# Optimization experiments

Hardware: AMD Instinct MI355X
Metric: run time of the kernel (lower is better)

## Reference

```python
import jax, jax.numpy as jnp
import numpy as np
import math

E = 1024   # embed_dim
H = 16     # num_heads
LAT = 1024 # latent_dim
P = LAT // 16  # projectionMatrice output dim (per-head width)
B = 2
S = 2048


def setup_inputs() -> dict:
    key = jax.random.key(0)
    ks = jax.random.split(key, 11)
    sc = 0.02  # small init scale so exp(dot(q_vec, k_vec)) stays finite
    return {
        "x": jax.random.normal(ks[0], (B, S, E), jnp.float32),
        "WQ": jax.random.normal(ks[1], (E, E), jnp.float32) * sc,
        "WK": jax.random.normal(ks[2], (E, E), jnp.float32) * sc,
        "WV": jax.random.normal(ks[3], (E, E), jnp.float32) * sc,
        "result_weight": jax.random.normal(ks[4], (E, E), jnp.float32) * sc,
        "proj_w": jax.random.normal(ks[5], (E, P), jnp.float32) * sc,
        "proj_b": jax.random.normal(ks[6], (P,), jnp.float32) * sc,
        "q1_vector": jax.random.normal(ks[7], (E,), jnp.float32) * sc,
        "k1_vector": jax.random.normal(ks[8], (E,), jnp.float32) * sc,
        "q2_vector": jax.random.normal(ks[9], (E,), jnp.float32) * sc,
        "k2_vector": jax.random.normal(ks[10], (E,), jnp.float32) * sc,
        "lambda_init": jnp.zeros((1,), jnp.float32),
    }


def reference(x, WQ, WK, WV, result_weight, proj_w, proj_b,
              q1_vector, k1_vector, q2_vector, k2_vector, lambda_init):
    head_dim = E // H
    scale = 1.0 / math.sqrt(head_dim)
    # projectionMatrice(x @ W): torch Linear -> x @ proj_w + proj_b with proj_w [E, P]
    q = (x @ WQ) @ proj_w + proj_b   # [B, S, P]
    k = (x @ WK) @ proj_w + proj_b   # [B, S, P]
    v = (x @ WV) @ proj_w + proj_b   # [B, S, P]
    q1, q2 = jnp.split(q, 2, axis=-1)  # [B, S, P/2] each
    k1, k2 = jnp.split(k, 2, axis=-1)
    lam = (jnp.exp(jnp.dot(q1_vector, k1_vector))
           - jnp.exp(jnp.dot(q2_vector, k2_vector)) + lambda_init[0])
    attn1 = jnp.einsum('bsp,btp->bst', q1, k1) * scale  # [B, S, S]
    attn2 = jnp.einsum('bsp,btp->bst', q2, k2) * scale
    base = jnp.einsum('bst,btp->bsp', attn1 - lam * attn2, v)  # [B, S, P]
    # Stateful KV-cache grows by one identical (key, value) copy per head call;
    # head i's tiled-cache output equals (i+1) * base (exact reassociation).
    mult = jnp.arange(1, H + 1, dtype=x.dtype)  # [H]
    heads = (base[:, :, None, :] * mult[None, None, :, None]).reshape(B, S, H * P)  # [B, S, E]
    return heads @ result_weight
```

## Files before the change

kernel.cpp:

```cpp
#include <hip/hip_runtime.h>
#include <hip/hip_bf16.h>


typedef __attribute__((ext_vector_type(8))) short short8;
typedef __attribute__((ext_vector_type(4))) float f32x4;
typedef unsigned short ushort_t;
typedef unsigned int uint_t;

__device__ inline ushort_t f2bf(float v) {
    uint_t u = __float_as_uint(v);
    return (ushort_t)((u + 0x7FFF + ((u >> 16) & 1)) >> 16);
}
__device__ inline float bf2f(ushort_t h) { return __uint_as_float(((uint_t)h) << 16); }
__device__ inline void split2(float v, ushort_t& hi, ushort_t& lo) {
    hi = f2bf(v);
    lo = f2bf(v - bf2f(hi));
}
__device__ inline int swzA(int row, int k) { return (row * 64 + k) ^ ((row & 7) << 3); }

__global__ __launch_bounds__(256) void prep2(
    const float* __restrict__ WQ, const float* __restrict__ WK, const float* __restrict__ WV,
    const float* __restrict__ proj_w, const float* __restrict__ RW,
    const float* __restrict__ q1v, const float* __restrict__ k1v,
    const float* __restrict__ q2v, const float* __restrict__ k2v,
    const float* __restrict__ lam0,
    ushort_t* __restrict__ WpThi, ushort_t* __restrict__ WpTlo,
    float* __restrict__ Weff, float* __restrict__ lamOut)
{
    int bid = blockIdx.x, tid = threadIdx.x;
    if (bid < 48) {
        __shared__ __align__(16) ushort_t Ah[4096], Al[4096], Bh[4096], Bl[4096];
        int z = bid >> 4, icb = bid & 15;
        const float* Wz = (z == 0) ? WQ : (z == 1) ? WK : WV;
        int i0 = icb * 64;
        int wave = tid >> 6, lane = tid & 63, rl = lane & 15, kg = lane >> 4;
        f32x4 acc[4] = {};
        float4 av[4], bv[4];
        #pragma unroll
        for (int i = 0; i < 4; ++i) {
            int pos = tid + 256 * i;
            int r = pos >> 4, c4 = (pos & 15) * 4;
            av[i] = *(const float4*)&proj_w[(long long)r * 64 + c4];
            bv[i] = *(const float4*)&Wz[(long long)(i0 + r) * 1024 + c4];
        }
        for (int ch = 0; ch < 16; ++ch) {
            #pragma unroll
            for (int i = 0; i < 4; ++i) {
                int pos = tid + 256 * i;
                int r = pos >> 4, c4 = (pos & 15) * 4;
                float va[4] = {av[i].x, av[i].y, av[i].z, av[i].w};
                #pragma unroll
                for (int j = 0; j < 4; ++j) {
                    ushort_t h, l; split2(va[j], h, l);
                    int idx = swzA(c4 + j, r);
                    Ah[idx] = h; Al[idx] = l;
                }
                ushort4 h4, l4;
                split2(bv[i].x, h4.x, l4.x); split2(bv[i].y, h4.y, l4.y);
                split2(bv[i].z, h4.z, l4.z); split2(bv[i].w, h4.w, l4.w);
                int bi = swzA(r, c4);
                *(ushort4*)&Bh[bi] = h4;
                *(ushort4*)&Bl[bi] = l4;
            }
            __syncthreads();
            if (ch < 15) {
                int k0 = (ch + 1) * 64;
                #pragma unroll
                for (int i = 0; i < 4; ++i) {
                    int pos = tid + 256 * i;
                    int r = pos >> 4, c4 = (pos & 15) * 4;
                    av[i] = *(const float4*)&proj_w[(long long)(k0 + r) * 64 + c4];
                    bv[i] = *(const float4*)&Wz[(long long)(i0 + r) * 1024 + k0 + c4];
                }
            }
            int ar = wave * 16 + rl;
            #pragma unroll
            for (int ks = 0; ks < 2; ++ks) {
                int kb = ks * 32 + kg * 8;
                short8 ah = *(const short8*)&Ah[swzA(ar, kb)];
                short8 al = *(const short8*)&Al[swzA(ar, kb)];
                #pragma unroll
                for (int n = 0; n < 4; ++n) {
                    int bi = swzA(n * 16 + rl, kb);
                    short8 bh = *(const short8*)&Bh[bi];
                    short8 bl = *(const short8*)&Bl[bi];
                    acc[n] = __builtin_amdgcn_mfma_f32_16x16x32_bf16(ah, bh, acc[n], 0, 0, 0);
                    acc[n] = __builtin_amdgcn_mfma_f32_16x16x32_bf16(ah, bl, acc[n], 0, 0, 0);
                    acc[n] = __builtin_amdgcn_mfma_f32_16x16x32_bf16(al, bh, acc[n], 0, 0, 0);
                }
            }
            __builtin_amdgcn_s_barrier();
        }
        #pragma unroll
        for (int n = 0; n < 4; ++n) {
            int icol = i0 + n * 16 + rl;
            #pragma unroll
            for (int j = 0; j < 4; ++j) {
                int prow = wave * 16 + kg * 4 + j;
                ushort_t h, l; split2(acc[n][j], h, l);
                long long idx = (long long)(z * 64 + prow) * 1024 + icol;
                WpThi[idx] = h; WpTlo[idx] = l;
            }
        }
    } else if (bid < 112) {
        int f4i = (bid - 48) * 256 + tid;
        int p = f4i >> 8, e4 = (f4i & 255) * 4;
        float4 s = {0.f, 0.f, 0.f, 0.f};
        #pragma unroll
        for (int h = 0; h < 16; ++h) {
            float4 r = *(const float4*)&RW[(long long)(h * 64 + p) * 1024 + e4];
            float m = (float)(h + 1);
            s.x += m * r.x; s.y += m * r.y; s.z += m * r.z; s.w += m * r.w;
        }
        *(float4*)&Weff[(long long)p * 1024 + e4] = s;
    } else {
        __shared__ float red[2][4];
        float d1 = 0.f, d2 = 0.f;
        for (int i = tid; i < 1024; i += 256) {
            d1 += q1v[i] * k1v[i];
            d2 += q2v[i] * k2v[i];
        }
        #pragma unroll
        for (int off = 32; off > 0; off >>= 1) {
            d1 += __shfl_down(d1, off);
            d2 += __shfl_down(d2, off);
        }
        int wave = tid >> 6;
        if ((tid & 63) == 0) { red[0][wave] = d1; red[1][wave] = d2; }
        __syncthreads();
        if (tid == 0) {
            float s1 = red[0][0] + red[0][1] + red[0][2] + red[0][3];
            float s2 = red[1][0] + red[1][1] + red[1][2] + red[1][3];
            *lamOut = expf(s1) - expf(s2) + lam0[0];
        }
    }
}

__global__ __launch_bounds__(256) void qkv2(
    const float* __restrict__ x,
    const ushort_t* __restrict__ WpThi, const ushort_t* __restrict__ WpTlo,
    const float* __restrict__ proj_b,
    ushort_t* __restrict__ Qhi, ushort_t* __restrict__ Qlo,
    float* __restrict__ kbuf, float* __restrict__ vbuf)
{
    __shared__ __align__(16) ushort_t Ah[4096], Al[4096], Bh[4096], Bl[4096];
    int bid = blockIdx.x, tid = threadIdx.x;
    int z = bid >> 6, rowblk = bid & 63;
    long long row0 = (long long)rowblk * 64;
    int wave = tid >> 6, lane = tid & 63, rl = lane & 15, kg = lane >> 4;
    f32x4 acc[4] = {};
    float4 av[4];
    short8 pbh[2], pbl[2];
    #pragma unroll
    for (int i = 0; i < 4; ++i) {
        int pos = tid + 256 * i;
        int r = pos >> 4, c4 = (pos & 15) * 4;
        av[i] = *(const float4*)&x[(row0 + r) * 1024 + c4];
    }
    #pragma unroll
    for (int i = 0; i < 2; ++i) {
        int pos = tid + 256 * i;
        int n = pos >> 3, k8 = (pos & 7) * 8;
        long long src = (long long)(z * 64 + n) * 1024 + k8;
        pbh[i] = *(const short8*)&WpThi[src];
        pbl[i] = *(const short8*)&WpTlo[src];
    }
    for (int ch = 0; ch < 16; ++ch) {
        #pragma unroll
        for (int i = 0; i < 4; ++i) {
            int pos = tid + 256 * i;
            int r = pos >> 4, c4 = (pos & 15) * 4;
            ushort4 h, l;
            split2(av[i].x, h.x, l.x); split2(av[i].y, h.y, l.y);
            split2(av[i].z, h.z, l.z); split2(av[i].w, h.w, l.w);
            int idx = swzA(r, c4);
            *(ushort4*)&Ah[idx] = h;
            *(ushort4*)&Al[idx] = l;
        }
        #pragma unroll
        for (int i = 0; i < 2; ++i) {
            int pos = tid + 256 * i;
            int n = pos >> 3, k8 = (pos & 7) * 8;
            int idx = swzA(n, k8);
            *(short8*)&Bh[idx] = pbh[i];
            *(short8*)&Bl[idx] = pbl[i];
        }
        __syncthreads();
        if (ch < 15) {
            int k0 = (ch + 1) * 64;
            #pragma unroll
            for (int i = 0; i < 4; ++i) {
                int pos = tid + 256 * i;
                int r = pos >> 4, c4 = (pos & 15) * 4;
                av[i] = *(const float4*)&x[(row0 + r) * 1024 + k0 + c4];
            }
            #pragma unroll
            for (int i = 0; i < 2; ++i) {
                int pos = tid + 256 * i;
                int n = pos >> 3, k8 = (pos & 7) * 8;
                long long src = (long long)(z * 64 + n) * 1024 + k0 + k8;
                pbh[i] = *(const short8*)&WpThi[src];
                pbl[i] = *(const short8*)&WpTlo[src];
            }
        }
        int ar = wave * 16 + rl;
        #pragma unroll
        for (int ks = 0; ks < 2; ++ks) {
            int kb = ks * 32 + kg * 8;
            short8 ah = *(const short8*)&Ah[swzA(ar, kb)];
            short8 al = *(const short8*)&Al[swzA(ar, kb)];
            #pragma unroll
            for (int n = 0; n < 4; ++n) {
                int bi = swzA(n * 16 + rl, kb);
                short8 bh = *(const short8*)&Bh[bi];
                short8 bl = *(const short8*)&Bl[bi];
                acc[n] = __builtin_amdgcn_mfma_f32_16x16x32_bf16(ah, bh, acc[n], 0, 0, 0);
                acc[n] = __builtin_amdgcn_mfma_f32_16x16x32_bf16(ah, bl, acc[n], 0, 0, 0);
                acc[n] = __builtin_amdgcn_mfma_f32_16x16x32_bf16(al, bh, acc[n], 0, 0, 0);
            }
        }
        __builtin_amdgcn_s_barrier();
    }
    #pragma unroll
    for (int n = 0; n < 4; ++n) {
        int col = n * 16 + rl;
        float bb = proj_b[col];
        #pragma unroll
        for (int j = 0; j < 4; ++j) {
            long long row = row0 + wave * 16 + kg * 4 + j;
            float val = acc[n][j] + bb;
            if (z == 0) {
                ushort_t h, l; split2(val, h, l);
                Qhi[row * 64 + col] = h;
                Qlo[row * 64 + col] = l;
            } else if (z == 1) {
                kbuf[row * 64 + col] = val;
            } else {
                vbuf[row * 64 + col] = val;
            }
        }
    }
}

__global__ __launch_bounds__(256) void mpart2(
    const float* __restrict__ kbuf, const float* __restrict__ vbuf,
    float* __restrict__ Mpart)
{
    int bid = blockIdx.x;
    int sc = bid & 63, b = bid >> 6;
    __shared__ float ksh[32][68], vsh[32][68];
    int tid = threadIdx.x;
    long long row0 = (long long)b * 2048 + sc * 32;
    #pragma unroll
    for (int i = 0; i < 4; ++i) {
        int pos = tid + 256 * i;
        int arr = pos >> 9, rem = pos & 511;
        int r = rem >> 4, c4 = (rem & 15) * 4;
        const float* src = (arr ? vbuf : kbuf) + (row0 + r) * 64 + c4;
        float4 v = *(const float4*)src;
        if (arr == 0) *(float4*)&ksh[r][c4] = v;
        else          *(float4*)&vsh[r][c4] = v;
    }
    __syncthreads();
    int p = tid & 63, cg = tid >> 6;
    float acc[16] = {};
    for (int s = 0; s < 32; ++s) {
        float vv = vsh[s][p];
        float4 k0 = *(const float4*)&ksh[s][cg * 16];
        float4 k1 = *(const float4*)&ksh[s][cg * 16 + 4];
        float4 k2 = *(const float4*)&ksh[s][cg * 16 + 8];
        float4 k3 = *(const float4*)&ksh[s][cg * 16 + 12];
        acc[0] += k0.x * vv;  acc[1] += k0.y * vv;  acc[2] += k0.z * vv;  acc[3] += k0.w * vv;
        acc[4] += k1.x * vv;  acc[5] += k1.y * vv;  acc[6] += k1.z * vv;  acc[7] += k1.w * vv;
        acc[8] += k2.x * vv;  acc[9] += k2.y * vv;  acc[10] += k2.z * vv; acc[11] += k2.w * vv;
        acc[12] += k3.x * vv; acc[13] += k3.y * vv; acc[14] += k3.z * vv; acc[15] += k3.w * vv;
    }
    float* o = Mpart + ((long long)b * 64 + sc) * 4096;
    #pragma unroll
    for (int ci = 0; ci < 16; ++ci)
        o[(cg * 16 + ci) * 64 + p] = acc[ci];
}

__global__ __launch_bounds__(256) void meffk(
    const float* __restrict__ Mpart, const float* __restrict__ lamPtr,
    float* __restrict__ Meff)
{
    int idx = blockIdx.x * 256 + threadIdx.x;
    int b = idx >> 12, cp = idx & 4095, c = cp >> 6;
    const float* base = Mpart + (long long)b * 262144 + cp;
    float s = 0.f;
    #pragma unroll 8
    for (int sc = 0; sc < 64; ++sc) s += base[(long long)sc * 4096];
    float lam = *lamPtr;
    Meff[idx] = s * 0.125f * (c < 32 ? 1.0f : -lam);
}

__global__ __launch_bounds__(256) void gkern2(
    const float* __restrict__ Meff, const float* __restrict__ Weff,
    ushort_t* __restrict__ GThi, ushort_t* __restrict__ GTlo)
{
    int colblk = blockIdx.x & 15, b = blockIdx.x >> 4;
    __shared__ float As[64][68];
    __shared__ float Bs[64][68];
    int tid = threadIdx.x;
    #pragma unroll
    for (int i = 0; i < 4; ++i) {
        int pos = tid + 256 * i;
        int c = pos >> 4, p4 = (pos & 15) * 4;
        *(float4*)&As[c][p4] = *(const float4*)&Meff[(long long)b * 4096 + c * 64 + p4];
    }
    #pragma unroll
    for (int i = 0; i < 4; ++i) {
        int pos = tid + 256 * i;
        int kk = pos >> 4, n4 = (pos & 15) * 4;
        *(float4*)&Bs[kk][n4] = *(const float4*)&Weff[(long long)kk * 1024 + colblk * 64 + n4];
    }
    __syncthreads();

    int tx = tid & 15, ty = tid >> 4;
    float acc[4][4] = {};
    #pragma unroll 4
    for (int kk4 = 0; kk4 < 64; kk4 += 4) {
        float4 a4[4], b4[4];
        #pragma unroll
        for (int i = 0; i < 4; ++i) a4[i] = *(const float4*)&As[ty * 4 + i][kk4];
        #pragma unroll
        for (int r = 0; r < 4; ++r) b4[r] = *(const float4*)&Bs[kk4 + r][tx * 4];
        #pragma unroll
        for (int i = 0; i < 4; ++i) {
            acc[i][0] += a4[i].x * b4[0].x + a4[i].y * b4[1].x + a4[i].z * b4[2].x + a4[i].w * b4[3].x;
            acc[i][1] += a4[i].x * b4[0].y + a4[i].y * b4[1].y + a4[i].z * b4[2].y + a4[i].w * b4[3].y;
            acc[i][2] += a4[i].x * b4[0].z + a4[i].y * b4[1].z + a4[i].z * b4[2].z + a4[i].w * b4[3].z;
            acc[i][3] += a4[i].x * b4[0].w + a4[i].y * b4[1].w + a4[i].z * b4[2].w + a4[i].w * b4[3].w;
        }
    }
    #pragma unroll
    for (int i = 0; i < 4; ++i)
        #pragma unroll
        for (int j = 0; j < 4; ++j) {
            ushort_t h, l; split2(acc[i][j], h, l);
            long long idx = (long long)b * 65536 + (long long)(colblk * 64 + tx * 4 + j) * 64 + ty * 4 + i;
            GThi[idx] = h; GTlo[idx] = l;
        }
}

__global__ __launch_bounds__(256) void outk(
    const ushort_t* __restrict__ Qhi, const ushort_t* __restrict__ Qlo,
    const ushort_t* __restrict__ GThi, const ushort_t* __restrict__ GTlo,
    float* __restrict__ out)
{
    __shared__ __align__(16) ushort_t Ah[4096], Al[4096], Bh[4096], Bl[4096];
    int bid = blockIdx.x;
    int rowblk = bid & 31, colblk = (bid >> 5) & 15, b = bid >> 9;
    int tid = threadIdx.x;
    long long row0 = (long long)b * 2048 + rowblk * 64;

    #pragma unroll
    for (int i = 0; i < 2; ++i) {
        int pos = tid + 256 * i;
        int n = pos >> 3, k8 = (pos & 7) * 8;
        int idx = swzA(n, k8);
        long long qsrc = (row0 + n) * 64 + k8;
        long long gsrc = (long long)b * 65536 + (long long)(colblk * 64 + n) * 64 + k8;
        *(short8*)&Ah[idx] = *(const short8*)&Qhi[qsrc];
        *(short8*)&Al[idx] = *(const short8*)&Qlo[qsrc];
        *(short8*)&Bh[idx] = *(const short8*)&GThi[gsrc];
        *(short8*)&Bl[idx] = *(const short8*)&GTlo[gsrc];
    }
    __syncthreads();

    int wave = tid >> 6, lane = tid & 63;
    int rl = lane & 15, kg = lane >> 4;
    f32x4 acc[4] = {};
    int ar = wave * 16 + rl;
    #pragma unroll
    for (int ks = 0; ks < 2; ++ks) {
        int kb = ks * 32 + kg * 8;
        short8 ah = *(const short8*)&Ah[swzA(ar, kb)];
        short8 al = *(const short8*)&Al[swzA(ar, kb)];
        #pragma unroll
        for (int n = 0; n < 4; ++n) {
            int bi = swzA(n * 16 + rl, kb);
            short8 bh = *(const short8*)&Bh[bi];
            short8 bl = *(const short8*)&Bl[bi];
            acc[n] = __builtin_amdgcn_mfma_f32_16x16x32_bf16(ah, bh, acc[n], 0, 0, 0);
            acc[n] = __builtin_amdgcn_mfma_f32_16x16x32_bf16(ah, bl, acc[n], 0, 0, 0);
            acc[n] = __builtin_amdgcn_mfma_f32_16x16x32_bf16(al, bh, acc[n], 0, 0, 0);
        }
    }
    #pragma unroll
    for (int n = 0; n < 4; ++n) {
        int col = colblk * 64 + n * 16 + rl;
        #pragma unroll
        for (int j = 0; j < 4; ++j) {
            int row = rowblk * 64 + wave * 16 + kg * 4 + j;
            out[(long long)b * 2097152 + (long long)row * 1024 + col] = acc[n][j];
        }
    }
}

extern "C" void kernel_launch(void* const* d_in, const int* in_sizes, int n_in,
                              void* d_out, int out_size, void* d_ws, size_t ws_size,
                              hipStream_t stream)
{
    const float* x      = (const float*)d_in[0];
    const float* WQ     = (const float*)d_in[1];
    const float* WK     = (const float*)d_in[2];
    const float* WV     = (const float*)d_in[3];
    const float* RW     = (const float*)d_in[4];
    const float* proj_w = (const float*)d_in[5];
    const float* proj_b = (const float*)d_in[6];
    const float* q1v    = (const float*)d_in[7];
    const float* k1v    = (const float*)d_in[8];
    const float* q2v    = (const float*)d_in[9];
    const float* k2v    = (const float*)d_in[10];
    const float* lam0   = (const float*)d_in[11];
    float* out = (float*)d_out;

    float* ws    = (float*)d_ws;
    float* kbuf  = ws;
    float* vbuf  = ws + 262144;
    float* Mpart = ws + 524288;
    float* Weff  = ws + 1048576;
    float* Meff  = ws + 1114112;
    float* lam   = ws + 1122304;
    ushort_t* ub = (ushort_t*)(ws + 1122320);
    ushort_t* WpThi = ub;
    ushort_t* WpTlo = ub + 196608;
    ushort_t* Qhi   = ub + 393216;
    ushort_t* Qlo   = ub + 655360;
    ushort_t* GThi  = ub + 917504;
    ushort_t* GTlo  = ub + 1048576;

    dim3 blk(256);
    prep2<<<dim3(113), blk, 0, stream>>>(WQ, WK, WV, proj_w, RW,
                                         q1v, k1v, q2v, k2v, lam0,
                                         WpThi, WpTlo, Weff, lam);
    qkv2<<<dim3(192), blk, 0, stream>>>(x, WpThi, WpTlo, proj_b, Qhi, Qlo, kbuf, vbuf);
    mpart2<<<dim3(128), blk, 0, stream>>>(kbuf, vbuf, Mpart);
    meffk<<<dim3(32), blk, 0, stream>>>(Mpart, lam, Meff);
    gkern2<<<dim3(32), blk, 0, stream>>>(Meff, Weff, GThi, GTlo);
    outk<<<dim3(1024), blk, 0, stream>>>(Qhi, Qlo, GThi, GTlo, out);
}
```

Baseline: 74.42 us.

## Fuse K/V projection with KᵀV partials and fold reductions into G kernel

The pipeline shrinks from six kernels to four. The K and V projections now share one block that computes both from the same staged x tile, then forms the 64-row KᵀV partial directly from shared memory instead of writing k/v buffers to global memory. The meff reduction, lambda computation and Weff head-sum move into the G kernel, and prep3 transposes proj_w through shared memory with double-buffered W loads. This cuts launches and global round trips, but leaves the Q projection on 64 blocks with half the work of the K/V blocks and recomputes Weff and lambda in every G block.

Measured after the change: 112.7 us. 1.51x slower.

```diff
diff --git a/kernel.cpp b/kernel.cpp
--- a/kernel.cpp
+++ b/kernel.cpp
@@ -18,191 +18,73 @@
 }
 __device__ inline int swzA(int row, int k) { return (row * 64 + k) ^ ((row & 7) << 3); }
 
-__global__ __launch_bounds__(256) void prep2(
+__global__ __launch_bounds__(256) void prep3(
     const float* __restrict__ WQ, const float* __restrict__ WK, const float* __restrict__ WV,
-    const float* __restrict__ proj_w, const float* __restrict__ RW,
-    const float* __restrict__ q1v, const float* __restrict__ k1v,
-    const float* __restrict__ q2v, const float* __restrict__ k2v,
-    const float* __restrict__ lam0,
-    ushort_t* __restrict__ WpThi, ushort_t* __restrict__ WpTlo,
-    float* __restrict__ Weff, float* __restrict__ lamOut)
+    const float* __restrict__ proj_w,
+    ushort_t* __restrict__ WpThi, ushort_t* __restrict__ WpTlo)
 {
+    __shared__ __align__(16) char smem[50176];
+    float (*At)[68] = (float(*)[68])smem;
+    ushort_t* Ah = (ushort_t*)(smem + 17408);
+    ushort_t* Al = (ushort_t*)(smem + 25600);
+    ushort_t* Bh = (ushort_t*)(smem + 33792);
+    ushort_t* Bl = (ushort_t*)(smem + 41984);
+
     int bid = blockIdx.x, tid = threadIdx.x;
-    if (bid < 48) {
-        __shared__ __align__(16) ushort_t Ah[4096], Al[4096], Bh[4096], Bl[4096];
-        int z = bid >> 4, icb = bid & 15;
-        const float* Wz = (z == 0) ? WQ : (z == 1) ? WK : WV;
-        int i0 = icb * 64;
-        int wave = tid >> 6, lane = tid & 63, rl = lane & 15, kg = lane >> 4;
-        f32x4 acc[4] = {};
-        float4 av[4], bv[4];
-        #pragma unroll
-        for (int i = 0; i < 4; ++i) {
-            int pos = tid + 256 * i;
-            int r = pos >> 4, c4 = (pos & 15) * 4;
-            av[i] = *(const float4*)&proj_w[(long long)r * 64 + c4];
-            bv[i] = *(const float4*)&Wz[(long long)(i0 + r) * 1024 + c4];
-        }
-        for (int ch = 0; ch < 16; ++ch) {
-            #pragma unroll
-            for (int i = 0; i < 4; ++i) {
-                int pos = tid + 256 * i;
-                int r = pos >> 4, c4 = (pos & 15) * 4;
-                float va[4] = {av[i].x, av[i].y, av[i].z, av[i].w};
-                #pragma unroll
-                for (int j = 0; j < 4; ++j) {
-                    ushort_t h, l; split2(va[j], h, l);
-                    int idx = swzA(c4 + j, r);
-                    Ah[idx] = h; Al[idx] = l;
-                }
-                ushort4 h4, l4;
-                split2(bv[i].x, h4.x, l4.x); split2(bv[i].y, h4.y, l4.y);
-                split2(bv[i].z, h4.z, l4.z); split2(bv[i].w, h4.w, l4.w);
-                int bi = swzA(r, c4);
-                *(ushort4*)&Bh[bi] = h4;
-                *(ushort4*)&Bl[bi] = l4;
-            }
-            __syncthreads();
-            if (ch < 15) {
-                int k0 = (ch + 1) * 64;
-                #pragma unroll
-                for (int i = 0; i < 4; ++i) {
-                    int pos = tid + 256 * i;
-                    int r = pos >> 4, c4 = (pos & 15) * 4;
-                    av[i] = *(const float4*)&proj_w[(long long)(k0 + r) * 64 + c4];
-                    bv[i] = *(const float4*)&Wz[(long long)(i0 + r) * 1024 + k0 + c4];
-                }
-            }
-            int ar = wave * 16 + rl;
-            #pragma unroll
-            for (int ks = 0; ks < 2; ++ks) {
-                int kb = ks * 32 + kg * 8;
-                short8 ah = *(const short8*)&Ah[swzA(ar, kb)];
-                short8 al = *(const short8*)&Al[swzA(ar, kb)];
-                #pragma unroll
-                for (int n = 0; n < 4; ++n) {
-                    int bi = swzA(n * 16 + rl, kb);
-                    short8 bh = *(const short8*)&Bh[bi];
-                    short8 bl = *(const short8*)&Bl[bi];
-                    acc[n] = __builtin_amdgcn_mfma_f32_16x16x32_bf16(ah, bh, acc[n], 0, 0, 0);
-                    acc[n] = __builtin_amdgcn_mfma_f32_16x16x32_bf16(ah, bl, acc[n], 0, 0, 0);
-                    acc[n] = __builtin_amdgcn_mfma_f32_16x16x32_bf16(al, bh, acc[n], 0, 0, 0);
-                }
-            }
-            __builtin_amdgcn_s_barrier();
-        }
-        #pragma unroll
-        for (int n = 0; n < 4; ++n) {
-            int icol = i0 + n * 16 + rl;
-            #pragma unroll
-            for (int j = 0; j < 4; ++j) {
-                int prow = wave * 16 + kg * 4 + j;
-                ushort_t h, l; split2(acc[n][j], h, l);
-                long long idx = (long long)(z * 64 + prow) * 1024 + icol;
-                WpThi[idx] = h; WpTlo[idx] = l;
-            }
-        }
-    } else if (bid < 112) {
-        int f4i = (bid - 48) * 256 + tid;
-        int p = f4i >> 8, e4 = (f4i & 255) * 4;
-        float4 s = {0.f, 0.f, 0.f, 0.f};
-        #pragma unroll
-        for (int h = 0; h < 16; ++h) {
-            float4 r = *(const float4*)&RW[(long long)(h * 64 + p) * 1024 + e4];
-            float m = (float)(h + 1);
-            s.x += m * r.x; s.y += m * r.y; s.z += m * r.z; s.w += m * r.w;
-        }
-        *(float4*)&Weff[(long long)p * 1024 + e4] = s;
-    } else {
-        __shared__ float red[2][4];
-        float d1 = 0.f, d2 = 0.f;
-        for (int i = tid; i < 1024; i += 256) {
-            d1 += q1v[i] * k1v[i];
-            d2 += q2v[i] * k2v[i];
-        }
-        #pragma unroll
-        for (int off = 32; off > 0; off >>= 1) {
-            d1 += __shfl_down(d1, off);
-            d2 += __shfl_down(d2, off);
-        }
-        int wave = tid >> 6;
-        if ((tid & 63) == 0) { red[0][wave] = d1; red[1][wave] = d2; }
-        __syncthreads();
-        if (tid == 0) {
-            float s1 = red[0][0] + red[0][1] + red[0][2] + red[0][3];
-            float s2 = red[1][0] + red[1][1] + red[1][2] + red[1][3];
-            *lamOut = expf(s1) - expf(s2) + lam0[0];
-        }
-    }
-}
-
-__global__ __launch_bounds__(256) void qkv2(
-    const float* __restrict__ x,
-    const ushort_t* __restrict__ WpThi, const ushort_t* __restrict__ WpTlo,
-    const float* __restrict__ proj_b,
-    ushort_t* __restrict__ Qhi, ushort_t* __restrict__ Qlo,
-    float* __restrict__ kbuf, float* __restrict__ vbuf)
-{
-    __shared__ __align__(16) ushort_t Ah[4096], Al[4096], Bh[4096], Bl[4096];
-    int bid = blockIdx.x, tid = threadIdx.x;
-    int z = bid >> 6, rowblk = bid & 63;
-    long long row0 = (long long)rowblk * 64;
+    int z = bid >> 4, jblk = bid & 15;
+    const float* Wz = (z == 0) ? WQ : (z == 1) ? WK : WV;
+    long long j0 = (long long)jblk * 64;
     int wave = tid >> 6, lane = tid & 63, rl = lane & 15, kg = lane >> 4;
     f32x4 acc[4] = {};
-    float4 av[4];
-    short8 pbh[2], pbl[2];
+
+    float4 av[4], bv0[4], bv1[4];
     #pragma unroll
     for (int i = 0; i < 4; ++i) {
         int pos = tid + 256 * i;
         int r = pos >> 4, c4 = (pos & 15) * 4;
-        av[i] = *(const float4*)&x[(row0 + r) * 1024 + c4];
-    }
-    #pragma unroll
-    for (int i = 0; i < 2; ++i) {
-        int pos = tid + 256 * i;
-        int n = pos >> 3, k8 = (pos & 7) * 8;
-        long long src = (long long)(z * 64 + n) * 1024 + k8;
-        pbh[i] = *(const short8*)&WpThi[src];
-        pbl[i] = *(const short8*)&WpTlo[src];
-    }
+        av[i]  = *(const float4*)&proj_w[(long long)r * 64 + c4];
+        bv0[i] = *(const float4*)&Wz[(j0 + r) * 1024 + c4];
+        bv1[i] = *(const float4*)&Wz[(j0 + r) * 1024 + 64 + c4];
+    }
+
     for (int ch = 0; ch < 16; ++ch) {
         #pragma unroll
         for (int i = 0; i < 4; ++i) {
             int pos = tid + 256 * i;
             int r = pos >> 4, c4 = (pos & 15) * 4;
+            *(float4*)&At[r][c4] = av[i];
             ushort4 h, l;
-            split2(av[i].x, h.x, l.x); split2(av[i].y, h.y, l.y);
-            split2(av[i].z, h.z, l.z); split2(av[i].w, h.w, l.w);
+            split2(bv0[i].x, h.x, l.x); split2(bv0[i].y, h.y, l.y);
+            split2(bv0[i].z, h.z, l.z); split2(bv0[i].w, h.w, l.w);
             int idx = swzA(r, c4);
-            *(ushort4*)&Ah[idx] = h;
-            *(ushort4*)&Al[idx] = l;
+            *(ushort4*)&Bh[idx] = h;
+            *(ushort4*)&Bl[idx] = l;
+        }
+        __syncthreads();
+        #pragma unroll
+        for (int i = 0; i < 4; ++i) {
+            int pos = tid + 256 * i;
+            int r = pos >> 4, c4 = (pos & 15) * 4;
+            if (ch < 15) av[i] = *(const float4*)&proj_w[(long long)((ch + 1) * 64 + r) * 64 + c4];
+            bv0[i] = bv1[i];
+            if (ch < 14) bv1[i] = *(const float4*)&Wz[(j0 + r) * 1024 + (ch + 2) * 64 + c4];
         }
         #pragma unroll
         for (int i = 0; i < 2; ++i) {
             int pos = tid + 256 * i;
-            int n = pos >> 3, k8 = (pos & 7) * 8;
-            int idx = swzA(n, k8);
-            *(short8*)&Bh[idx] = pbh[i];
-            *(short8*)&Bl[idx] = pbl[i];
+            int p = pos & 63, d8 = pos >> 6;
+            short8 h8, l8;
+            #pragma unroll
+            for (int t = 0; t < 8; ++t) {
+                ushort_t hh, ll;
+                split2(At[d8 * 8 + t][p], hh, ll);
+                h8[t] = (short)hh; l8[t] = (short)ll;
+            }
+            int idx = swzA(p, d8 * 8);
+            *(short8*)&Ah[idx] = h8;
+            *(short8*)&Al[idx] = l8;
         }
         __syncthreads();
-        if (ch < 15) {
-            int k0 = (ch + 1) * 64;
-            #pragma unroll
-            for (int i = 0; i < 4; ++i) {
-                int pos = tid + 256 * i;
-                int r = pos >> 4, c4 = (pos & 15) * 4;
-                av[i] = *(const float4*)&x[(row0 + r) * 1024 + k0 + c4];
-            }
-            #pragma unroll
-            for (int i = 0; i < 2; ++i) {
-                int pos = tid + 256 * i;
-                int n = pos >> 3, k8 = (pos & 7) * 8;
-                long long src = (long long)(z * 64 + n) * 1024 + k0 + k8;
-                pbh[i] = *(const short8*)&WpThi[src];
-                pbl[i] = *(const short8*)&WpTlo[src];
-            }
-        }
         int ar = wave * 16 + rl;
         #pragma unroll
         for (int ks = 0; ks < 2; ++ks) {
@@ -223,97 +105,235 @@
     }
     #pragma unroll
     for (int n = 0; n < 4; ++n) {
-        int col = n * 16 + rl;
-        float bb = proj_b[col];
+        long long jcol = j0 + n * 16 + rl;
         #pragma unroll
         for (int j = 0; j < 4; ++j) {
-            long long row = row0 + wave * 16 + kg * 4 + j;
-            float val = acc[n][j] + bb;
-            if (z == 0) {
-                ushort_t h, l; split2(val, h, l);
+            int prow = wave * 16 + kg * 4 + j;
+            ushort_t h, l; split2(acc[n][j], h, l);
+            long long idx = (long long)(z * 64 + prow) * 1024 + jcol;
+            WpThi[idx] = h; WpTlo[idx] = l;
+        }
+    }
+}
+
+__global__ __launch_bounds__(256) void qkv3(
+    const float* __restrict__ x,
+    const ushort_t* __restrict__ WpThi, const ushort_t* __restrict__ WpTlo,
+    const float* __restrict__ proj_b,
+    ushort_t* __restrict__ Qhi, ushort_t* __restrict__ Qlo,
+    float* __restrict__ Mpart)
+{
+    __shared__ __align__(16) char smem[49152];
+    ushort_t* Ah  = (ushort_t*)(smem);
+    ushort_t* Al  = (ushort_t*)(smem + 8192);
+    ushort_t* B1h = (ushort_t*)(smem + 16384);
+    ushort_t* B1l = (ushort_t*)(smem + 24576);
+    ushort_t* B2h = (ushort_t*)(smem + 32768);
+    ushort_t* B2l = (ushort_t*)(smem + 40960);
+    float (*ksh)[68] = (float(*)[68])(smem);
+    float (*vsh)[68] = (float(*)[68])(smem + 17408);
+
+    int bid = blockIdx.x, tid = threadIdx.x;
+    int kv = bid >> 6, rowblk = bid & 63;
+    long long row0 = (long long)rowblk * 64;
+    int wave = tid >> 6, lane = tid & 63, rl = lane & 15, kg = lane >> 4;
+    int zb1 = kv ? 64 : 0;
+
+    f32x4 acc1[4] = {}, acc2[4] = {};
+    float4 av0[4], av1[4];
+    short8 p1h[2], p1l[2], p2h[2], p2l[2];
+
+    #pragma unroll
+    for (int i = 0; i < 4; ++i) {
+        int pos = tid + 256 * i;
+        int r = pos >> 4, c4 = (pos & 15) * 4;
+        av0[i] = *(const float4*)&x[(row0 + r) * 1024 + c4];
+        av1[i] = *(const float4*)&x[(row0 + r) * 1024 + 64 + c4];
+    }
+    #pragma unroll
+    for (int i = 0; i < 2; ++i) {
+        int pos = tid + 256 * i;
+        int n = pos >> 3, k8 = (pos & 7) * 8;
+        p1h[i] = *(const short8*)&WpThi[(long long)(zb1 + n) * 1024 + k8];
+        p1l[i] = *(const short8*)&WpTlo[(long long)(zb1 + n) * 1024 + k8];
+        if (kv) {
+            p2h[i] = *(const short8*)&WpThi[(long long)(128 + n) * 1024 + k8];
+            p2l[i] = *(const short8*)&WpTlo[(long long)(128 + n) * 1024 + k8];
+        }
+    }
+
+    for (int ch = 0; ch < 16; ++ch) {
+        #pragma unroll
+        for (int i = 0; i < 4; ++i) {
+            int pos = tid + 256 * i;
+            int r = pos >> 4, c4 = (pos & 15) * 4;
+            ushort4 h, l;
+            split2(av0[i].x, h.x, l.x); split2(av0[i].y, h.y, l.y);
+            split2(av0[i].z, h.z, l.z); split2(av0[i].w, h.w, l.w);
+            int idx = swzA(r, c4);
+            *(ushort4*)&Ah[idx] = h;
+            *(ushort4*)&Al[idx] = l;
+        }
+        #pragma unroll
+        for (int i = 0; i < 2; ++i) {
+            int pos = tid + 256 * i;
+            int n = pos >> 3, k8 = (pos & 7) * 8;
+            int idx = swzA(n, k8);
+            *(short8*)&B1h[idx] = p1h[i];
+            *(short8*)&B1l[idx] = p1l[i];
+            if (kv) {
+                *(short8*)&B2h[idx] = p2h[i];
+                *(short8*)&B2l[idx] = p2l[i];
+            }
+        }
+        __syncthreads();
+        #pragma unroll
+        for (int i = 0; i < 4; ++i) {
+            int pos = tid + 256 * i;
+            int r = pos >> 4, c4 = (pos & 15) * 4;
+            av0[i] = av1[i];
+            if (ch < 14) av1[i] = *(const float4*)&x[(row0 + r) * 1024 + (ch + 2) * 64 + c4];
+        }
+        if (ch < 15) {
+            int k0n = (ch + 1) * 64;
+            #pragma unroll
+            for (int i = 0; i < 2; ++i) {
+                int pos = tid + 256 * i;
+                int n = pos >> 3, k8 = (pos & 7) * 8;
+                p1h[i] = *(const short8*)&WpThi[(long long)(zb1 + n) * 1024 + k0n + k8];
+                p1l[i] = *(const short8*)&WpTlo[(long long)(zb1 + n) * 1024 + k0n + k8];
+                if (kv) {
+                    p2h[i] = *(const short8*)&WpThi[(long long)(128 + n) * 1024 + k0n + k8];
+                    p2l[i] = *(const short8*)&WpTlo[(long long)(128 + n) * 1024 + k0n + k8];
+                }
+            }
+        }
+        int ar = wave * 16 + rl;
+        #pragma unroll
+        for (int ks = 0; ks < 2; ++ks) {
+            int kb = ks * 32 + kg * 8;
+            short8 ah = *(const short8*)&Ah[swzA(ar, kb)];
+            short8 al = *(const short8*)&Al[swzA(ar, kb)];
+            #pragma unroll
+            for (int n = 0; n < 4; ++n) {
+                int bi = swzA(n * 16 + rl, kb);
+                short8 bh = *(const short8*)&B1h[bi];
+                short8 bl = *(const short8*)&B1l[bi];
+                acc1[n] = __builtin_amdgcn_mfma_f32_16x16x32_bf16(ah, bh, acc1[n], 0, 0, 0);
+                acc1[n] = __builtin_amdgcn_mfma_f32_16x16x32_bf16(ah, bl, acc1[n], 0, 0, 0);
+                acc1[n] = __builtin_amdgcn_mfma_f32_16x16x32_bf16(al, bh, acc1[n], 0, 0, 0);
+                if (kv) {
+                    short8 ch2 = *(const short8*)&B2h[bi];
+                    short8 cl2 = *(const short8*)&B2l[bi];
+                    acc2[n] = __builtin_amdgcn_mfma_f32_16x16x32_bf16(ah, ch2, acc2[n], 0, 0, 0);
+                    acc2[n] = __builtin_amdgcn_mfma_f32_16x16x32_bf16(ah, cl2, acc2[n], 0, 0, 0);
+                    acc2[n] = __builtin_amdgcn_mfma_f32_16x16x32_bf16(al, ch2, acc2[n], 0, 0, 0);
+                }
+            }
+        }
+        __builtin_amdgcn_s_barrier();
+    }
+
+    if (!kv) {
+        #pragma unroll
+        for (int n = 0; n < 4; ++n) {
+            int col = n * 16 + rl;
+            float bb = proj_b[col];
+            #pragma unroll
+            for (int j = 0; j < 4; ++j) {
+                long long row = row0 + wave * 16 + kg * 4 + j;
+                ushort_t h, l; split2(acc1[n][j] + bb, h, l);
                 Qhi[row * 64 + col] = h;
                 Qlo[row * 64 + col] = l;
-            } else if (z == 1) {
-                kbuf[row * 64 + col] = val;
-            } else {
-                vbuf[row * 64 + col] = val;
-            }
-        }
-    }
-}
-
-__global__ __launch_bounds__(256) void mpart2(
-    const float* __restrict__ kbuf, const float* __restrict__ vbuf,
-    float* __restrict__ Mpart)
-{
-    int bid = blockIdx.x;
-    int sc = bid & 63, b = bid >> 6;
-    __shared__ float ksh[32][68], vsh[32][68];
-    int tid = threadIdx.x;
-    long long row0 = (long long)b * 2048 + sc * 32;
-    #pragma unroll
-    for (int i = 0; i < 4; ++i) {
-        int pos = tid + 256 * i;
-        int arr = pos >> 9, rem = pos & 511;
-        int r = rem >> 4, c4 = (rem & 15) * 4;
-        const float* src = (arr ? vbuf : kbuf) + (row0 + r) * 64 + c4;
-        float4 v = *(const float4*)src;
-        if (arr == 0) *(float4*)&ksh[r][c4] = v;
-        else          *(float4*)&vsh[r][c4] = v;
-    }
-    __syncthreads();
-    int p = tid & 63, cg = tid >> 6;
-    float acc[16] = {};
-    for (int s = 0; s < 32; ++s) {
-        float vv = vsh[s][p];
-        float4 k0 = *(const float4*)&ksh[s][cg * 16];
-        float4 k1 = *(const float4*)&ksh[s][cg * 16 + 4];
-        float4 k2 = *(const float4*)&ksh[s][cg * 16 + 8];
-        float4 k3 = *(const float4*)&ksh[s][cg * 16 + 12];
-        acc[0] += k0.x * vv;  acc[1] += k0.y * vv;  acc[2] += k0.z * vv;  acc[3] += k0.w * vv;
-        acc[4] += k1.x * vv;  acc[5] += k1.y * vv;  acc[6] += k1.z * vv;  acc[7] += k1.w * vv;
-        acc[8] += k2.x * vv;  acc[9] += k2.y * vv;  acc[10] += k2.z * vv; acc[11] += k2.w * vv;
-        acc[12] += k3.x * vv; acc[13] += k3.y * vv; acc[14] += k3.z * vv; acc[15] += k3.w * vv;
-    }
-    float* o = Mpart + ((long long)b * 64 + sc) * 4096;
-    #pragma unroll
-    for (int ci = 0; ci < 16; ++ci)
-        o[(cg * 16 + ci) * 64 + p] = acc[ci];
-}
-
-__global__ __launch_bounds__(256) void meffk(
-    const float* __restrict__ Mpart, const float* __restrict__ lamPtr,
-    float* __restrict__ Meff)
-{
-    int idx = blockIdx.x * 256 + threadIdx.x;
-    int b = idx >> 12, cp = idx & 4095, c = cp >> 6;
-    const float* base = Mpart + (long long)b * 262144 + cp;
-    float s = 0.f;
-    #pragma unroll 8
-    for (int sc = 0; sc < 64; ++sc) s += base[(long long)sc * 4096];
-    float lam = *lamPtr;
-    Meff[idx] = s * 0.125f * (c < 32 ? 1.0f : -lam);
-}
-
-__global__ __launch_bounds__(256) void gkern2(
-    const float* __restrict__ Meff, const float* __restrict__ Weff,
+            }
+        }
+    } else {
+        #pragma unroll
+        for (int n = 0; n < 4; ++n) {
+            int col = n * 16 + rl;
+            float bb = proj_b[col];
+            #pragma unroll
+            for (int j = 0; j < 4; ++j) {
+                int r = wave * 16 + kg * 4 + j;
+                ksh[r][col] = acc1[n][j] + bb;
+                vsh[r][col] = acc2[n][j] + bb;
+            }
+        }
+        __syncthreads();
+        int p = tid & 63, cg = tid >> 6;
+        float macc[16] = {};
+        for (int s = 0; s < 64; ++s) {
+            float vv = vsh[s][p];
+            float4 k0 = *(const float4*)&ksh[s][cg * 16];
+            float4 k1 = *(const float4*)&ksh[s][cg * 16 + 4];
+            float4 k2 = *(const float4*)&ksh[s][cg * 16 + 8];
+            float4 k3 = *(const float4*)&ksh[s][cg * 16 + 12];
+            macc[0] += k0.x * vv;  macc[1] += k0.y * vv;  macc[2] += k0.z * vv;  macc[3] += k0.w * vv;
+            macc[4] += k1.x * vv;  macc[5] += k1.y * vv;  macc[6] += k1.z * vv;  macc[7] += k1.w * vv;
+            macc[8] += k2.x * vv;  macc[9] += k2.y * vv;  macc[10] += k2.z * vv; macc[11] += k2.w * vv;
+            macc[12] += k3.x * vv; macc[13] += k3.y * vv; macc[14] += k3.z * vv; macc[15] += k3.w * vv;
+        }
+        float* o = Mpart + (long long)rowblk * 4096;
+        #pragma unroll
+        for (int ci = 0; ci < 16; ++ci)
+            o[(cg * 16 + ci) * 64 + p] = macc[ci];
+    }
+}
+
+__global__ __launch_bounds__(256) void gkern3(
+    const float* __restrict__ Mpart, const float* __restrict__ RW,
+    const float* __restrict__ q1v, const float* __restrict__ k1v,
+    const float* __restrict__ q2v, const float* __restrict__ k2v,
+    const float* __restrict__ lam0,
     ushort_t* __restrict__ GThi, ushort_t* __restrict__ GTlo)
 {
     int colblk = blockIdx.x & 15, b = blockIdx.x >> 4;
-    __shared__ float As[64][68];
-    __shared__ float Bs[64][68];
+    __shared__ float As[64][68], Bs[64][68];
+    __shared__ float red[2][4];
     int tid = threadIdx.x;
+
+    float d1 = 0.f, d2 = 0.f;
+    for (int i = tid; i < 1024; i += 256) {
+        d1 += q1v[i] * k1v[i];
+        d2 += q2v[i] * k2v[i];
+    }
+    #pragma unroll
+    for (int off = 32; off > 0; off >>= 1) {
+        d1 += __shfl_down(d1, off);
+        d2 += __shfl_down(d2, off);
+    }
+    if ((tid & 63) == 0) { red[0][tid >> 6] = d1; red[1][tid >> 6] = d2; }
+    __syncthreads();
+    float s1 = red[0][0] + red[0][1] + red[0][2] + red[0][3];
+    float s2 = red[1][0] + red[1][1] + red[1][2] + red[1][3];
+    float lam = expf(s1) - expf(s2) + lam0[0];
+
     #pragma unroll
     for (int i = 0; i < 4; ++i) {
         int pos = tid + 256 * i;
         int c = pos >> 4, p4 = (pos & 15) * 4;
-        *(float4*)&As[c][p4] = *(const float4*)&Meff[(long long)b * 4096 + c * 64 + p4];
+        float4 s = {0.f, 0.f, 0.f, 0.f};
+        #pragma unroll 8
+        for (int sc = 0; sc < 32; ++sc) {
+            float4 m = *(const float4*)&Mpart[(long long)(b * 32 + sc) * 4096 + c * 64 + p4];
+            s.x += m.x; s.y += m.y; s.z += m.z; s.w += m.w;
+        }
+        float coef = 0.125f * (c < 32 ? 1.0f : -lam);
+        s.x *= coef; s.y *= coef; s.z *= coef; s.w *= coef;
+        *(float4*)&As[c][p4] = s;
     }
     #pragma unroll
     for (int i = 0; i < 4; ++i) {
         int pos = tid + 256 * i;
-        int kk = pos >> 4, n4 = (pos & 15) * 4;
-        *(float4*)&Bs[kk][n4] = *(const float4*)&Weff[(long long)kk * 1024 + colblk * 64 + n4];
+        int p = pos >> 4, e4 = (pos & 15) * 4;
+        float4 s = {0.f, 0.f, 0.f, 0.f};
+        #pragma unroll
+        for (int h = 0; h < 16; ++h) {
+            float4 r = *(const float4*)&RW[(long long)(h * 64 + p) * 1024 + colblk * 64 + e4];
+            float m = (float)(h + 1);
+            s.x += m * r.x; s.y += m * r.y; s.z += m * r.z; s.w += m * r.w;
+        }
+        *(float4*)&Bs[p][e4] = s;
     }
     __syncthreads();
 
@@ -418,13 +438,8 @@
     float* out = (float*)d_out;
 
     float* ws    = (float*)d_ws;
-    float* kbuf  = ws;
-    float* vbuf  = ws + 262144;
-    float* Mpart = ws + 524288;
-    float* Weff  = ws + 1048576;
-    float* Meff  = ws + 1114112;
-    float* lam   = ws + 1122304;
-    ushort_t* ub = (ushort_t*)(ws + 1122320);
+    float* Mpart = ws;
+    ushort_t* ub = (ushort_t*)(ws + 262144);
     ushort_t* WpThi = ub;
     ushort_t* WpTlo = ub + 196608;
     ushort_t* Qhi   = ub + 393216;
@@ -433,12 +448,8 @@
     ushort_t* GTlo  = ub + 1048576;
 
     dim3 blk(256);
-    prep2<<<dim3(113), blk, 0, stream>>>(WQ, WK, WV, proj_w, RW,
-                                         q1v, k1v, q2v, k2v, lam0,
-                                         WpThi, WpTlo, Weff, lam);
-    qkv2<<<dim3(192), blk, 0, stream>>>(x, WpThi, WpTlo, proj_b, Qhi, Qlo, kbuf, vbuf);
-    mpart2<<<dim3(128), blk, 0, stream>>>(kbuf, vbuf, Mpart);
-    meffk<<<dim3(32), blk, 0, stream>>>(Mpart, lam, Meff);
-    gkern2<<<dim3(32), blk, 0, stream>>>(Meff, Weff, GThi, GTlo);
+    prep3<<<dim3(48), blk, 0, stream>>>(WQ, WK, WV, proj_w, WpThi, WpTlo);
+    qkv3<<<dim3(128), blk, 0, stream>>>(x, WpThi, WpTlo, proj_b, Qhi, Qlo, Mpart);
+    gkern3<<<dim3(32), blk, 0, stream>>>(Mpart, RW, q1v, k1v, q2v, k2v, lam0, GThi, GTlo);
     outk<<<dim3(1024), blk, 0, stream>>>(Qhi, Qlo, GThi, GTlo, out);
 }
```

## Split-K the weight-projection prep and fold Meff/Weff/lambda into gkern

Applied to the files above, without the earlier changes.

The W@proj_w precompute is split across 8 K-slices (384 blocks instead of 48), which write fp32 partials that a new reduction kernel sums and converts to hi/lo bf16. The Mpart reduction, the Weff head-weighted sum of result_weight and the lambda dot products move into the gkern kernel, removing the meffk launch and the Weff/Meff round trips. This targets the long serial 16-chunk loop in the 48-block prep kernel. In exchange it adds extra partial-buffer traffic, one more launch, and redundant lambda and Weff recomputation in each of the 32 gkern blocks.

Result: faster. 70.34 us (-5.5%).

```diff
diff --git a/kernel.cpp b/kernel.cpp
--- a/kernel.cpp
+++ b/kernel.cpp
@@ -18,122 +18,93 @@
 }
 __device__ inline int swzA(int row, int k) { return (row * 64 + k) ^ ((row & 7) << 3); }
 
-__global__ __launch_bounds__(256) void prep2(
+__global__ __launch_bounds__(256) void prep_sk(
     const float* __restrict__ WQ, const float* __restrict__ WK, const float* __restrict__ WV,
-    const float* __restrict__ proj_w, const float* __restrict__ RW,
-    const float* __restrict__ q1v, const float* __restrict__ k1v,
-    const float* __restrict__ q2v, const float* __restrict__ k2v,
-    const float* __restrict__ lam0,
-    ushort_t* __restrict__ WpThi, ushort_t* __restrict__ WpTlo,
-    float* __restrict__ Weff, float* __restrict__ lamOut)
-{
-    int bid = blockIdx.x, tid = threadIdx.x;
-    if (bid < 48) {
-        __shared__ __align__(16) ushort_t Ah[4096], Al[4096], Bh[4096], Bl[4096];
-        int z = bid >> 4, icb = bid & 15;
-        const float* Wz = (z == 0) ? WQ : (z == 1) ? WK : WV;
-        int i0 = icb * 64;
-        int wave = tid >> 6, lane = tid & 63, rl = lane & 15, kg = lane >> 4;
-        f32x4 acc[4] = {};
-        float4 av[4], bv[4];
+    const float* __restrict__ proj_w, float* __restrict__ wppartT)
+{
+    __shared__ __align__(16) ushort_t Ah[4096], Al[4096], Bh[4096], Bl[4096];
+    int bid = blockIdx.x;
+    int slice = bid / 48, t = bid % 48, z = t / 16, rowblk = t % 16;
+    const float* A = ((z == 0) ? WQ : (z == 1) ? WK : WV) + (long long)rowblk * 64 * 1024;
+
+    int tid = threadIdx.x;
+    int wave = tid >> 6, lane = tid & 63;
+    int rl = lane & 15, kg = lane >> 4;
+    f32x4 acc[4] = {};
+
+    int k0 = slice * 128;
+    for (int ch = 0; ch < 2; ++ch, k0 += 64) {
         #pragma unroll
         for (int i = 0; i < 4; ++i) {
             int pos = tid + 256 * i;
-            int r = pos >> 4, c4 = (pos & 15) * 4;
-            av[i] = *(const float4*)&proj_w[(long long)r * 64 + c4];
-            bv[i] = *(const float4*)&Wz[(long long)(i0 + r) * 1024 + c4];
-        }
-        for (int ch = 0; ch < 16; ++ch) {
-            #pragma unroll
-            for (int i = 0; i < 4; ++i) {
-                int pos = tid + 256 * i;
-                int r = pos >> 4, c4 = (pos & 15) * 4;
-                float va[4] = {av[i].x, av[i].y, av[i].z, av[i].w};
-                #pragma unroll
-                for (int j = 0; j < 4; ++j) {
-                    ushort_t h, l; split2(va[j], h, l);
-                    int idx = swzA(c4 + j, r);
-                    Ah[idx] = h; Al[idx] = l;
-                }
-                ushort4 h4, l4;
-                split2(bv[i].x, h4.x, l4.x); split2(bv[i].y, h4.y, l4.y);
-                split2(bv[i].z, h4.z, l4.z); split2(bv[i].w, h4.w, l4.w);
-                int bi = swzA(r, c4);
-                *(ushort4*)&Bh[bi] = h4;
-                *(ushort4*)&Bl[bi] = l4;
-            }
-            __syncthreads();
-            if (ch < 15) {
-                int k0 = (ch + 1) * 64;
-                #pragma unroll
-                for (int i = 0; i < 4; ++i) {
-                    int pos = tid + 256 * i;
-                    int r = pos >> 4, c4 = (pos & 15) * 4;
-                    av[i] = *(const float4*)&proj_w[(long long)(k0 + r) * 64 + c4];
-                    bv[i] = *(const float4*)&Wz[(long long)(i0 + r) * 1024 + k0 + c4];
-                }
-            }
-            int ar = wave * 16 + rl;
-            #pragma unroll
-            for (int ks = 0; ks < 2; ++ks) {
-                int kb = ks * 32 + kg * 8;
-                short8 ah = *(const short8*)&Ah[swzA(ar, kb)];
-                short8 al = *(const short8*)&Al[swzA(ar, kb)];
-                #pragma unroll
-                for (int n = 0; n < 4; ++n) {
-                    int bi = swzA(n * 16 + rl, kb);
-                    short8 bh = *(const short8*)&Bh[bi];
-                    short8 bl = *(const short8*)&Bl[bi];
-                    acc[n] = __builtin_amdgcn_mfma_f32_16x16x32_bf16(ah, bh, acc[n], 0, 0, 0);
-                    acc[n] = __builtin_amdgcn_mfma_f32_16x16x32_bf16(ah, bl, acc[n], 0, 0, 0);
-                    acc[n] = __builtin_amdgcn_mfma_f32_16x16x32_bf16(al, bh, acc[n], 0, 0, 0);
-                }
-            }
-            __builtin_amdgcn_s_barrier();
-        }
-        #pragma unroll
-        for (int n = 0; n < 4; ++n) {
-            int icol = i0 + n * 16 + rl;
+            int r = pos >> 4, k4 = (pos & 15) * 4;
+            float4 v = *(const float4*)&A[(long long)r * 1024 + k0 + k4];
+            ushort4 h, l;
+            split2(v.x, h.x, l.x); split2(v.y, h.y, l.y);
+            split2(v.z, h.z, l.z); split2(v.w, h.w, l.w);
+            int idx = swzA(r, k4);
+            *(ushort4*)&Ah[idx] = h;
+            *(ushort4*)&Al[idx] = l;
+        }
+        #pragma unroll
+        for (int i = 0; i < 4; ++i) {
+            int pos = tid + 256 * i;
+            int kk = pos >> 4, n4 = (pos & 15) * 4;
+            float4 v = *(const float4*)&proj_w[(long long)(k0 + kk) * 64 + n4];
+            float vv[4] = {v.x, v.y, v.z, v.w};
             #pragma unroll
             for (int j = 0; j < 4; ++j) {
-                int prow = wave * 16 + kg * 4 + j;
-                ushort_t h, l; split2(acc[n][j], h, l);
-                long long idx = (long long)(z * 64 + prow) * 1024 + icol;
-                WpThi[idx] = h; WpTlo[idx] = l;
-            }
-        }
-    } else if (bid < 112) {
-        int f4i = (bid - 48) * 256 + tid;
-        int p = f4i >> 8, e4 = (f4i & 255) * 4;
-        float4 s = {0.f, 0.f, 0.f, 0.f};
-        #pragma unroll
-        for (int h = 0; h < 16; ++h) {
-            float4 r = *(const float4*)&RW[(long long)(h * 64 + p) * 1024 + e4];
-            float m = (float)(h + 1);
-            s.x += m * r.x; s.y += m * r.y; s.z += m * r.z; s.w += m * r.w;
-        }
-        *(float4*)&Weff[(long long)p * 1024 + e4] = s;
-    } else {
-        __shared__ float red[2][4];
-        float d1 = 0.f, d2 = 0.f;
-        for (int i = tid; i < 1024; i += 256) {
-            d1 += q1v[i] * k1v[i];
-            d2 += q2v[i] * k2v[i];
-        }
-        #pragma unroll
-        for (int off = 32; off > 0; off >>= 1) {
-            d1 += __shfl_down(d1, off);
-            d2 += __shfl_down(d2, off);
-        }
-        int wave = tid >> 6;
-        if ((tid & 63) == 0) { red[0][wave] = d1; red[1][wave] = d2; }
+                ushort_t h, l; split2(vv[j], h, l);
+                int idx = swzA(n4 + j, kk);
+                Bh[idx] = h; Bl[idx] = l;
+            }
+        }
         __syncthreads();
-        if (tid == 0) {
-            float s1 = red[0][0] + red[0][1] + red[0][2] + red[0][3];
-            float s2 = red[1][0] + red[1][1] + red[1][2] + red[1][3];
-            *lamOut = expf(s1) - expf(s2) + lam0[0];
-        }
-    }
+        int ar = wave * 16 + rl;
+        #pragma unroll
+        for (int ks = 0; ks < 2; ++ks) {
+            int kb = ks * 32 + kg * 8;
+            short8 ah = *(const short8*)&Ah[swzA(ar, kb)];
+            short8 al = *(const short8*)&Al[swzA(ar, kb)];
+            #pragma unroll
+            for (int n = 0; n < 4; ++n) {
+                int bi = swzA(n * 16 + rl, kb);
+                short8 bh = *(const short8*)&Bh[bi];
+                short8 bl = *(const short8*)&Bl[bi];
+                acc[n] = __builtin_amdgcn_mfma_f32_16x16x32_bf16(ah, bh, acc[n], 0, 0, 0);
+                acc[n] = __builtin_amdgcn_mfma_f32_16x16x32_bf16(ah, bl, acc[n], 0, 0, 0);
+                acc[n] = __builtin_amdgcn_mfma_f32_16x16x32_bf16(al, bh, acc[n], 0, 0, 0);
+            }
+        }
+        __syncthreads();
+    }
+    #pragma unroll
+    for (int n = 0; n < 4; ++n) {
+        int col = n * 16 + rl;
+        float4 o = {acc[n][0], acc[n][1], acc[n][2], acc[n][3]};
+        long long idx = (long long)slice * 196608 + (long long)(z * 64 + col) * 1024
+                      + rowblk * 64 + wave * 16 + kg * 4;
+        *(float4*)&wppartT[idx] = o;
+    }
+}
+
+__global__ __launch_bounds__(256) void wpfix2(
+    const float* __restrict__ wppartT,
+    ushort_t* __restrict__ WpThi, ushort_t* __restrict__ WpTlo)
+{
+    int idx = blockIdx.x * 256 + threadIdx.x;
+    long long off = (long long)idx * 4;
+    float4 s = {0.f, 0.f, 0.f, 0.f};
+    #pragma unroll
+    for (int sl = 0; sl < 8; ++sl) {
+        float4 m = *(const float4*)&wppartT[(long long)sl * 196608 + off];
+        s.x += m.x; s.y += m.y; s.z += m.z; s.w += m.w;
+    }
+    ushort4 h, l;
+    split2(s.x, h.x, l.x); split2(s.y, h.y, l.y);
+    split2(s.z, h.z, l.z); split2(s.w, h.w, l.w);
+    *(ushort4*)&WpThi[off] = h;
+    *(ushort4*)&WpTlo[off] = l;
 }
 
 __global__ __launch_bounds__(256) void qkv2(
@@ -281,39 +252,60 @@
         o[(cg * 16 + ci) * 64 + p] = acc[ci];
 }
 
-__global__ __launch_bounds__(256) void meffk(
-    const float* __restrict__ Mpart, const float* __restrict__ lamPtr,
-    float* __restrict__ Meff)
-{
-    int idx = blockIdx.x * 256 + threadIdx.x;
-    int b = idx >> 12, cp = idx & 4095, c = cp >> 6;
-    const float* base = Mpart + (long long)b * 262144 + cp;
-    float s = 0.f;
-    #pragma unroll 8
-    for (int sc = 0; sc < 64; ++sc) s += base[(long long)sc * 4096];
-    float lam = *lamPtr;
-    Meff[idx] = s * 0.125f * (c < 32 ? 1.0f : -lam);
-}
-
-__global__ __launch_bounds__(256) void gkern2(
-    const float* __restrict__ Meff, const float* __restrict__ Weff,
+__global__ __launch_bounds__(256) void gkern3(
+    const float* __restrict__ Mpart, const float* __restrict__ RW,
+    const float* __restrict__ q1v, const float* __restrict__ k1v,
+    const float* __restrict__ q2v, const float* __restrict__ k2v,
+    const float* __restrict__ lam0,
     ushort_t* __restrict__ GThi, ushort_t* __restrict__ GTlo)
 {
     int colblk = blockIdx.x & 15, b = blockIdx.x >> 4;
-    __shared__ float As[64][68];
-    __shared__ float Bs[64][68];
+    __shared__ float As[64][68], Bs[64][68];
+    __shared__ float red[2][4];
     int tid = threadIdx.x;
+
+    float d1 = 0.f, d2 = 0.f;
+    for (int i = tid; i < 1024; i += 256) {
+        d1 += q1v[i] * k1v[i];
+        d2 += q2v[i] * k2v[i];
+    }
+    #pragma unroll
+    for (int off = 32; off > 0; off >>= 1) {
+        d1 += __shfl_down(d1, off);
+        d2 += __shfl_down(d2, off);
+    }
+    if ((tid & 63) == 0) { red[0][tid >> 6] = d1; red[1][tid >> 6] = d2; }
+    __syncthreads();
+    float s1 = red[0][0] + red[0][1] + red[0][2] + red[0][3];
+    float s2 = red[1][0] + red[1][1] + red[1][2] + red[1][3];
+    float lam = expf(s1) - expf(s2) + lam0[0];
+
     #pragma unroll
     for (int i = 0; i < 4; ++i) {
         int pos = tid + 256 * i;
         int c = pos >> 4, p4 = (pos & 15) * 4;
-        *(float4*)&As[c][p4] = *(const float4*)&Meff[(long long)b * 4096 + c * 64 + p4];
+        float4 s = {0.f, 0.f, 0.f, 0.f};
+        #pragma unroll 8
+        for (int sc = 0; sc < 64; ++sc) {
+            float4 m = *(const float4*)&Mpart[((long long)b * 64 + sc) * 4096 + c * 64 + p4];
+            s.x += m.x; s.y += m.y; s.z += m.z; s.w += m.w;
+        }
+        float coef = 0.125f * (c < 32 ? 1.0f : -lam);
+        s.x *= coef; s.y *= coef; s.z *= coef; s.w *= coef;
+        *(float4*)&As[c][p4] = s;
     }
     #pragma unroll
     for (int i = 0; i < 4; ++i) {
         int pos = tid + 256 * i;
-        int kk = pos >> 4, n4 = (pos & 15) * 4;
-        *(float4*)&Bs[kk][n4] = *(const float4*)&Weff[(long long)kk * 1024 + colblk * 64 + n4];
+        int p = pos >> 4, e4 = (pos & 15) * 4;
+        float4 s = {0.f, 0.f, 0.f, 0.f};
+        #pragma unroll
+        for (int h = 0; h < 16; ++h) {
+            float4 r = *(const float4*)&RW[(long long)(h * 64 + p) * 1024 + colblk * 64 + e4];
+            float m = (float)(h + 1);
+            s.x += m * r.x; s.y += m * r.y; s.z += m * r.z; s.w += m * r.w;
+        }
+        *(float4*)&Bs[p][e4] = s;
     }
     __syncthreads();
 
@@ -417,14 +409,12 @@
     const float* lam0   = (const float*)d_in[11];
     float* out = (float*)d_out;
 
-    float* ws    = (float*)d_ws;
-    float* kbuf  = ws;
-    float* vbuf  = ws + 262144;
-    float* Mpart = ws + 524288;
-    float* Weff  = ws + 1048576;
-    float* Meff  = ws + 1114112;
-    float* lam   = ws + 1122304;
-    ushort_t* ub = (ushort_t*)(ws + 1122320);
+    float* ws       = (float*)d_ws;
+    float* wppartT  = ws;
+    float* kbuf     = ws + 1572864;
+    float* vbuf     = ws + 1835008;
+    float* Mpart    = ws + 2097152;
+    ushort_t* ub    = (ushort_t*)(ws + 2621440);
     ushort_t* WpThi = ub;
     ushort_t* WpTlo = ub + 196608;
     ushort_t* Qhi   = ub + 393216;
@@ -433,12 +423,10 @@
     ushort_t* GTlo  = ub + 1048576;
 
     dim3 blk(256);
-    prep2<<<dim3(113), blk, 0, stream>>>(WQ, WK, WV, proj_w, RW,
-                                         q1v, k1v, q2v, k2v, lam0,
-                                         WpThi, WpTlo, Weff, lam);
+    prep_sk<<<dim3(384), blk, 0, stream>>>(WQ, WK, WV, proj_w, wppartT);
+    wpfix2<<<dim3(192), blk, 0, stream>>>(wppartT, WpThi, WpTlo);
     qkv2<<<dim3(192), blk, 0, stream>>>(x, WpThi, WpTlo, proj_b, Qhi, Qlo, kbuf, vbuf);
     mpart2<<<dim3(128), blk, 0, stream>>>(kbuf, vbuf, Mpart);
-    meffk<<<dim3(32), blk, 0, stream>>>(Mpart, lam, Meff);
-    gkern2<<<dim3(32), blk, 0, stream>>>(Meff, Weff, GThi, GTlo);
+    gkern3<<<dim3(32), blk, 0, stream>>>(Mpart, RW, q1v, k1v, q2v, k2v, lam0, GThi, GTlo);
     outk<<<dim3(1024), blk, 0, stream>>>(Qhi, Qlo, GThi, GTlo, out);
 }
```
